# Kernel tuning notes

Hardware: AMD Instinct MI355X
Metric: run time of the kernel (lower is better)

## Reference

```python
import jax, jax.numpy as jnp
import numpy as np

EPS = 1e-5
N_LAYERS = 4  # int(log2(patch_size=16))


def _conv(x, w, stride=1, pad=0):
    return jax.lax.conv_general_dilated(
        x, w, (stride, stride), ((pad, pad), (pad, pad)),
        dimension_numbers=('NCHW', 'OIHW', 'NCHW'))


def _mbn(x, m, g, b):
    # masked BatchNorm1d over active (nnz) sites only; m is [B,1,H,W] 0/1
    cnt = jnp.maximum(m.sum(), 1.0)
    mean = (x * m).sum((0, 2, 3)) / cnt
    xc = x - mean[None, :, None, None]
    var = (xc * xc * m).sum((0, 2, 3)) / cnt
    y = xc * jax.lax.rsqrt(var + EPS)[None, :, None, None]
    return (y * g[None, :, None, None] + b[None, :, None, None]) * m


def _down_mask(m):
    # active-output sites of a k=3, stride=2, pad=1 regular sparse conv
    return jax.lax.reduce_window(m, 0.0, jax.lax.max, (1, 1, 3, 3), (1, 1, 2, 2),
                                 ((0, 0), (0, 0), (1, 1), (1, 1)))


def setup_inputs() -> dict:
    key = jax.random.key(0)
    ks = jax.random.split(key, 24)
    B, C, H, W = 8, 3, 256, 256
    hd, ed, L = 192, 192, 256
    w = lambda k, shp: jax.random.normal(k, shp, jnp.float32) * 0.05
    inp = {
        'images': jax.random.normal(ks[0], (B, C, H, W), jnp.float32),
        'mask': jax.random.randint(ks[1], (B, L), 0, 2).astype(jnp.int32),
        'stem_w': w(ks[2], (hd, C, 1, 1)),
        'stem_g': jnp.ones((hd,), jnp.float32), 'stem_b': jnp.zeros((hd,), jnp.float32),
        'dw1': w(ks[3], (N_LAYERS, hd, hd, 3, 3)),
        'dg1': jnp.ones((N_LAYERS, hd), jnp.float32), 'db1': jnp.zeros((N_LAYERS, hd), jnp.float32),
        'dw2': w(ks[4], (N_LAYERS, hd, hd, 3, 3)),
        'dg2': jnp.ones((N_LAYERS, hd), jnp.float32), 'db2': jnp.zeros((N_LAYERS, hd), jnp.float32),
        'rw1': w(ks[5], (N_LAYERS, hd, hd, 3, 3)),
        'rg1': jnp.ones((N_LAYERS, hd), jnp.float32), 'rb1': jnp.zeros((N_LAYERS, hd), jnp.float32),
        'rw2': w(ks[6], (N_LAYERS, hd, hd, 3, 3)),
        'rg2': jnp.ones((N_LAYERS, hd), jnp.float32), 'rb2': jnp.zeros((N_LAYERS, hd), jnp.float32),
        'final_w': w(ks[7], (ed, hd, 1, 1)),
        'final_g': jnp.ones((ed,), jnp.float32), 'final_b': jnp.zeros((ed,), jnp.float32),
    }
    return inp


def reference(images, mask, stem_w, stem_g, stem_b,
              dw1, dg1, db1, dw2, dg2, db2,
              rw1, rg1, rb1, rw2, rg2, rb2,
              final_w, final_g, final_b):
    B, C, H, W = images.shape
    L = mask.shape[1]
    f = int(np.sqrt(L))
    s = H // f
    keep = (1 - mask).astype(images.dtype).reshape(B, f, f)
    m = jnp.repeat(jnp.repeat(keep, s, axis=1), s, axis=2)[:, None]  # [B,1,H,W]
    x = images * m  # dense emulation of sparse tensor: inactive sites are zero

    # stem (regular 1x1 conv, active set unchanged) + BN + ReLU
    x = jnp.maximum(_mbn(_conv(x, stem_w), m, stem_g, stem_b), 0.0)

    for i in range(N_LAYERS):
        # ResBlockDownSparse: regular conv k3 s2 -> BN -> ReLU -> subm conv -> BN
        x = _conv(x, dw1[i], stride=2, pad=1)
        m = _down_mask(m)
        x = jnp.maximum(_mbn(x, m, dg1[i], db1[i]), 0.0)
        x = _mbn(_conv(x, dw2[i], 1, 1), m, dg2[i], db2[i])
        # ResBlockSparse (in==out, no skip projection)
        idn = x
        h = jnp.maximum(_mbn(_conv(x, rw1[i], 1, 1), m, rg1[i], rb1[i]), 0.0)
        h = _mbn(_conv(h, rw2[i], 1, 1), m, rg2[i], rb2[i])
        x = jnp.maximum(h + idn, 0.0)

    # final 1x1 subm proj + BN + ReLU
    x = jnp.maximum(_mbn(_conv(x, final_w), m, final_g, final_b), 0.0)
    ids_restore = jnp.tile(jnp.arange(L, dtype=jnp.int32)[None], (B, 1))
    return x, mask, ids_restore
```

## Files before the change

### kernel.cpp

```cpp
#include <hip/hip_runtime.h>
#include <hip/hip_bf16.h>

typedef __hip_bfloat16 bf16;
typedef unsigned short u16;
typedef unsigned int u32;
typedef unsigned char u8;
typedef __attribute__((ext_vector_type(8))) short bf16x8;
typedef __attribute__((ext_vector_type(4))) float f32x4;

#define NB 8
#define CH 192
#define WSZ (CH*CH*9)
#define WBLK (CH*32)


static __device__ __forceinline__ float bf2f(bf16 v){ return __bfloat162float(v); }
static __device__ __forceinline__ u16 f2bu(float f){
  union { bf16 h; u16 u; } cv; cv.h = __float2bfloat16(f); return cv.u;
}
static __device__ __forceinline__ float u2f(u16 u){
  union { bf16 h; u16 u; } cv; cv.u = u; return __bfloat162float(cv.h);
}
static __device__ __forceinline__ u32 pk2bf(float a, float b){
  union { __hip_bfloat162 h; u32 u; } cv;
  cv.h = __float22bfloat162_rn(make_float2(a, b));
  return cv.u;
}

static __device__ __forceinline__ void build_ss(const float* __restrict__ stIn,
        const float* __restrict__ g, const float* __restrict__ bb,
        const float* __restrict__ cnt, float* scs, float* shs, int t){
  if(t < CH){
    float s = 0.f, s2 = 0.f;
#pragma unroll
    for(int b=0;b<NB;b++){ s += stIn[b*384 + t]; s2 += stIn[b*384 + 192 + t]; }
    float n = fmaxf(*cnt, 1.0f);
    float mean = s/n;
    float var = fmaxf(s2/n - mean*mean, 0.f);
    float rstd = rsqrtf(var + 1e-5f);
    float sc = g[t]*rstd;
    scs[t] = sc;
    shs[t] = bb[t] - mean*sc;
  }
}

template<int RELU>
static __device__ __forceinline__ uint4 affine8(uint4 v, const float* scp, const float* shp){
  float4 sa = *(const float4*)(scp);
  float4 sb = *(const float4*)(scp+4);
  float4 ha = *(const float4*)(shp);
  float4 hb = *(const float4*)(shp+4);
  u16* pv = (u16*)&v;
  float f0, f1;
  f0 = u2f(pv[0])*sa.x + ha.x; f1 = u2f(pv[1])*sa.y + ha.y;
  if(RELU){ f0 = fmaxf(f0,0.f); f1 = fmaxf(f1,0.f); }
  ((u32*)&v)[0] = pk2bf(f0, f1);
  f0 = u2f(pv[2])*sa.z + ha.z; f1 = u2f(pv[3])*sa.w + ha.w;
  if(RELU){ f0 = fmaxf(f0,0.f); f1 = fmaxf(f1,0.f); }
  ((u32*)&v)[1] = pk2bf(f0, f1);
  f0 = u2f(pv[4])*sb.x + hb.x; f1 = u2f(pv[5])*sb.y + hb.y;
  if(RELU){ f0 = fmaxf(f0,0.f); f1 = fmaxf(f1,0.f); }
  ((u32*)&v)[2] = pk2bf(f0, f1);
  f0 = u2f(pv[6])*sb.z + hb.z; f1 = u2f(pv[7])*sb.w + hb.w;
  if(RELU){ f0 = fmaxf(f0,0.f); f1 = fmaxf(f1,0.f); }
  ((u32*)&v)[3] = pk2bf(f0, f1);
  return v;
}


__global__ void k_zero(float* p, int n){
  int i = blockIdx.x*blockDim.x + threadIdx.x;
  if(i < n) p[i] = 0.f;
}

__global__ void k_fill(float* p, int n, float v){
  int i = blockIdx.x*blockDim.x + threadIdx.x;
  if(i < n) p[i] = v;
}

__global__ void k_mask0(const int* __restrict__ mask, u8* __restrict__ m0){
  int i = blockIdx.x*blockDim.x + threadIdx.x;
  if(i >= NB*65536) return;
  int b = i >> 16; int p = i & 65535;
  int y = p >> 8, x = p & 255;
  int patch = (y >> 4)*16 + (x >> 4);
  m0[i] = (u8)(1 - mask[b*256 + patch]);
}

__global__ void k_maskdown(const u8* __restrict__ mi, u8* __restrict__ mo,
                           int Ho, int Wo, int Hi, int Wi){
  int i = blockIdx.x*blockDim.x + threadIdx.x;
  int total = NB*Ho*Wo; if(i >= total) return;
  int b = i/(Ho*Wo); int p = i%(Ho*Wo);
  int oy = p/Wo, ox = p%Wo;
  u8 v = 0;
  for(int ky=0; ky<3; ky++){
    int iy = oy*2 + ky - 1; if(iy < 0 || iy >= Hi) continue;
    for(int kx=0; kx<3; kx++){
      int ix = ox*2 + kx - 1; if(ix < 0 || ix >= Wi) continue;
      u8 t = mi[(b*Hi + iy)*Wi + ix]; if(t > v) v = t;
    }
  }
  mo[i] = v;
}

__global__ void k_count(const u8* __restrict__ m, int n, float* cnt){
  int i = blockIdx.x*blockDim.x + threadIdx.x;
  int stride = gridDim.x*blockDim.x;
  int local = 0;
  for(int j=i; j<n; j+=stride) local += m[j];
  for(int o=32; o>0; o>>=1) local += __shfl_down(local, o, 64);
  if((threadIdx.x & 63) == 0 && local) atomicAdd(cnt, (float)local);
}


__global__ __launch_bounds__(256) void k_moments(const float* __restrict__ im,
        const u8* __restrict__ m0, float* __restrict__ mom){
  float s[9];
#pragma unroll
  for(int k=0;k<9;k++) s[k]=0.f;
  int stride = gridDim.x*blockDim.x;
  for(int i = blockIdx.x*blockDim.x + threadIdx.x; i < NB*65536; i += stride){
    if(m0[i]){
      int b = i >> 16, p = i & 65535;
      float r = im[(size_t)(b*3+0)*65536 + p];
      float g = im[(size_t)(b*3+1)*65536 + p];
      float bl= im[(size_t)(b*3+2)*65536 + p];
      s[0]+=r;    s[1]+=g;    s[2]+=bl;
      s[3]+=r*r;  s[4]+=g*g;  s[5]+=bl*bl;
      s[6]+=r*g;  s[7]+=r*bl; s[8]+=g*bl;
    }
  }
#pragma unroll
  for(int k=0;k<9;k++){
    for(int o=32; o>0; o>>=1) s[k] += __shfl_down(s[k], o, 64);
  }
  __shared__ float sh[4][9];
  int w = threadIdx.x >> 6;
  if((threadIdx.x & 63) == 0){
#pragma unroll
    for(int k=0;k<9;k++) sh[w][k] = s[k];
  }
  __syncthreads();
  if(threadIdx.x < 9){
    float tt = sh[0][threadIdx.x] + sh[1][threadIdx.x] + sh[2][threadIdx.x] + sh[3][threadIdx.x];
    atomicAdd(&mom[threadIdx.x], tt);
  }
}

__global__ void k_stemfinal(const float* __restrict__ mom, const float* __restrict__ cnt,
        const float* __restrict__ sw, const float* __restrict__ g,
        const float* __restrict__ bb, float* __restrict__ ssA){
  int c = threadIdx.x; if(c >= CH) return;
  float n = fmaxf(*cnt, 1.0f);
  float m0=mom[0], m1=mom[1], m2=mom[2], m3=mom[3], m4=mom[4];
  float m5=mom[5], m6=mom[6], m7=mom[7], m8=mom[8];
  float w0 = sw[c*3+0], w1 = sw[c*3+1], w2 = sw[c*3+2];
  float mean = (w0*m0 + w1*m1 + w2*m2)/n;
  float e2 = (w0*w0*m3 + w1*w1*m4 + w2*w2*m5
            + 2.f*(w0*w1*m6 + w0*w2*m7 + w1*w2*m8))/n;
  float var = fmaxf(e2 - mean*mean, 0.f);
  float sc = g[c]*rsqrtf(var + 1e-5f);
  ssA[c] = sc;
  ssA[CH + c] = bb[c] - mean*sc;
}

__global__ void k_fold(const float* __restrict__ sw, const float* __restrict__ ssA,
                       float* __restrict__ swf){
  int c = threadIdx.x; if(c >= CH) return;
  float sc = ssA[c];
  swf[c*4+0] = sc*sw[c*3+0];
  swf[c*4+1] = sc*sw[c*3+1];
  swf[c*4+2] = sc*sw[c*3+2];
  swf[c*4+3] = ssA[CH+c];
}

__global__ void k_repack16(const float* __restrict__ dw1, const float* __restrict__ dw2,
                           const float* __restrict__ rw1, const float* __restrict__ rw2,
                           bf16* __restrict__ wb){
  int i = blockIdx.x*blockDim.x + threadIdx.x;
  if(i >= 16*WSZ) return;
  int stage = i/(4*WSZ);
  int sel = (i/WSZ)%4;
  int r = i%WSZ;
  const float* w = (sel==0)?dw1 : (sel==1)?dw2 : (sel==2)?rw1 : rw2;
  float val = w[(size_t)stage*WSZ + r];
  int tap = r%9; int ci = (r/9)%CH; int co = r/(9*CH);
  wb[(size_t)(stage*4+sel)*WSZ + ((size_t)(tap*6 + (ci>>5))*CH + co)*32 + (ci&31)]
      = __float2bfloat16(val);
}

__global__ void k_repackF(const float* __restrict__ fw, bf16* __restrict__ wb){
  int i = blockIdx.x*blockDim.x + threadIdx.x;
  if(i >= CH*CH) return;
  int co = i/CH, ci = i%CH;
  wb[((size_t)(ci>>5)*CH + co)*32 + (ci&31)] = __float2bfloat16(fw[i]);
}


static __device__ __forceinline__ void epi_stats(f32x4 (&acc)[4][3], const u8* sm,
        float* __restrict__ statsB, int b, int co0, int l15, int q, int lane){
  float s[3], s2[3];
#pragma unroll
  for(int nt=0;nt<3;nt++){ s[nt]=0.f; s2[nt]=0.f; }
#pragma unroll
  for(int mt=0;mt<4;mt++){
#pragma unroll
    for(int r=0;r<4;r++){
      int site = mt*16 + q*4 + r;
      float mv = (float)sm[site];
#pragma unroll
      for(int nt=0;nt<3;nt++){
        float v = acc[mt][nt][r]*mv;
        s[nt] += v; s2[nt] += v*v;
      }
    }
  }
#pragma unroll
  for(int nt=0;nt<3;nt++){
    s[nt]  += __shfl_down(s[nt], 32, 64);  s[nt]  += __shfl_down(s[nt], 16, 64);
    s2[nt] += __shfl_down(s2[nt], 32, 64); s2[nt] += __shfl_down(s2[nt], 16, 64);
  }
  if(lane < 16){
#pragma unroll
    for(int nt=0;nt<3;nt++){
      int co = co0 + nt*16 + l15;
      atomicAdd(&statsB[b*384 + co], s[nt]);
      atomicAdd(&statsB[b*384 + 192 + co], s2[nt]);
    }
  }
}

static __device__ __forceinline__ void epi_store(f32x4 (&acc)[4][3], u16* obuf,
        u16* __restrict__ out, int b, int oy0, int ox0, int Ho, int Wo,
        int t, int co0, int l15, int q){
  __syncthreads();
#pragma unroll
  for(int mt=0;mt<4;mt++){
#pragma unroll
    for(int nt=0;nt<3;nt++){
      int co = co0 + nt*16 + l15;
#pragma unroll
      for(int r=0;r<4;r++){
        int site = mt*16 + q*4 + r;
        obuf[site*212 + co] = f2bu(acc[mt][nt][r]);
      }
    }
  }
  __syncthreads();
  for(int e=t; e<3072; e+=256){
    int r = e/384; int off = (e%384)*4;
    int sx = off/CH, co = off%CH;
    ushort4 v = *(const ushort4*)&obuf[(r*8+sx)*212 + co];
    *(ushort4*)(out + ((size_t)(b*Ho+oy0+r)*Wo + ox0)*CH + off) = v;
  }
}


static __device__ __forceinline__ void epi_stats8(f32x4 (&acc)[8][3], const u8* sm,
        float* __restrict__ statsB, int b, int co0, int l15, int q, int lane){
  float s[3], s2[3];
#pragma unroll
  for(int nt=0;nt<3;nt++){ s[nt]=0.f; s2[nt]=0.f; }
#pragma unroll
  for(int mt=0;mt<8;mt++){
#pragma unroll
    for(int r=0;r<4;r++){
      int site = mt*16 + q*4 + r;
      float mv = (float)sm[site];
#pragma unroll
      for(int nt=0;nt<3;nt++){
        float v = acc[mt][nt][r]*mv;
        s[nt] += v; s2[nt] += v*v;
      }
    }
  }
#pragma unroll
  for(int nt=0;nt<3;nt++){
    s[nt]  += __shfl_down(s[nt], 32, 64);  s[nt]  += __shfl_down(s[nt], 16, 64);
    s2[nt] += __shfl_down(s2[nt], 32, 64); s2[nt] += __shfl_down(s2[nt], 16, 64);
  }
  if(lane < 16){
#pragma unroll
    for(int nt=0;nt<3;nt++){
      int co = co0 + nt*16 + l15;
      atomicAdd(&statsB[b*384 + co], s[nt]);
      atomicAdd(&statsB[b*384 + 192 + co], s2[nt]);
    }
  }
}

static __device__ __forceinline__ void epi_store_q(f32x4 (&acc)[8][3], u16* obuf,
        u16* __restrict__ out, int b, int oy0, int ox0, int Ho, int Wo,
        int t, int co0, int l15, int q, int qd){
  __syncthreads();
#pragma unroll
  for(int mi=0; mi<2; mi++){
    int mt = qd*2 + mi;
#pragma unroll
    for(int nt=0;nt<3;nt++){
      int co = co0 + nt*16 + l15;
#pragma unroll
      for(int r=0;r<4;r++){
        int site = mi*16 + q*4 + r;
        obuf[site*212 + co] = f2bu(acc[mt][nt][r]);
      }
    }
  }
  __syncthreads();
  for(int e=t; e<1536; e+=256){
    int r = e/384; int off = (e%384)*4;
    int sx = off/CH, co = off%CH;
    ushort4 v = *(const ushort4*)&obuf[(r*8+sx)*212 + co];
    *(ushort4*)(out + ((size_t)(b*Ho+oy0+qd*4+r)*Wo + ox0)*CH + off) = v;
  }
}


static __device__ __forceinline__ void epi_statsT(f32x4 (&acc)[2][3], const u8* sm,
        float* __restrict__ statsB, int b, int co0, int l15, int q, int lane, int mh){
  float s[3], s2[3];
#pragma unroll
  for(int nt=0;nt<3;nt++){ s[nt]=0.f; s2[nt]=0.f; }
#pragma unroll
  for(int mt=0;mt<2;mt++){
#pragma unroll
    for(int r=0;r<4;r++){
      int site = mh*32 + mt*16 + q*4 + r;
      float mv = (float)sm[site];
#pragma unroll
      for(int nt=0;nt<3;nt++){
        float v = acc[mt][nt][r]*mv;
        s[nt] += v; s2[nt] += v*v;
      }
    }
  }
#pragma unroll
  for(int nt=0;nt<3;nt++){
    s[nt]  += __shfl_down(s[nt], 32, 64);  s[nt]  += __shfl_down(s[nt], 16, 64);
    s2[nt] += __shfl_down(s2[nt], 32, 64); s2[nt] += __shfl_down(s2[nt], 16, 64);
  }
  if(lane < 16){
#pragma unroll
    for(int nt=0;nt<3;nt++){
      int co = co0 + nt*16 + l15;
      atomicAdd(&statsB[b*384 + co], s[nt]);
      atomicAdd(&statsB[b*384 + 192 + co], s2[nt]);
    }
  }
}

static __device__ __forceinline__ void epi_storeT(f32x4 (&acc)[2][3], u16* obuf,
        u16* __restrict__ out, int b, int oy0, int ox0, int Ho, int Wo,
        int t, int w, int coh, int l15, int q, int mh){
  __syncthreads();
#pragma unroll
  for(int mt=0;mt<2;mt++){
#pragma unroll
    for(int nt=0;nt<3;nt++){
      int col = (w&1)*48 + nt*16 + l15;
#pragma unroll
      for(int r=0;r<4;r++){
        int site = mh*32 + mt*16 + q*4 + r;
        obuf[site*104 + col] = f2bu(acc[mt][nt][r]);
      }
    }
  }
  __syncthreads();
  for(int e=t; e<1536; e+=256){
    int site = e/24; int grp = e%24;
    ushort4 v = *(const ushort4*)&obuf[site*104 + grp*4];
    *(ushort4*)(out + ((size_t)(b*Ho+oy0+(site>>3))*Wo + ox0+(site&7))*CH + coh*96 + grp*4) = v;
  }
}

#define CIP 104
template<int RELU>
__global__ __launch_bounds__(256) void k_convm(const bf16* __restrict__ in,
        const bf16* __restrict__ wb, const u8* __restrict__ mk,
        bf16* __restrict__ out, int Ho, int Wo,
        const float* __restrict__ stIn, const float* __restrict__ gIn,
        const float* __restrict__ bIn, const float* __restrict__ cnt,
        float* __restrict__ statsB){
  __shared__ __align__(16) u16 tile[180*CIP];
  __shared__ __align__(16) float scs[CH], shs[CH];
  __shared__ u8 sm[128];
  __shared__ u8 wmk[180];
  __shared__ int anyact;
  const int t = threadIdx.x;
  const int b = blockIdx.z;
  const int ox0 = blockIdx.x*8, oy0 = blockIdx.y*16;
  const int gy0 = oy0 - 1, gx0 = ox0 - 1;

  if(t == 0) anyact = 0;
  __syncthreads();
  if(t < 128){
    int r = t >> 3, c = t & 7;
    u8 mv = mk[(b*Ho + oy0 + r)*Wo + ox0 + c];
    sm[t] = mv;
    if(mv) anyact = 1;
  }
  for(int e=t; e<180; e+=256){
    int y = e/10, x = e%10;
    int gy = gy0 + y, gx = gx0 + x;
    u8 mv = 0;
    if(gy >= 0 && gy < Ho && gx >= 0 && gx < Wo) mv = mk[(b*Ho+gy)*Wo+gx];
    wmk[e] = mv;
  }
  __syncthreads();
  if(!anyact) return;

  build_ss(stIn, gIn, bIn, cnt, scs, shs, t);
  __syncthreads();

  const u16* inp = (const u16*)in;
  const int w = t >> 6;
  const int l = t & 63;
  const int l15 = l & 15, q = l >> 4;
  f32x4 acc[8][3];
#pragma unroll
  for(int mt=0;mt<8;mt++)
#pragma unroll
    for(int nt=0;nt<3;nt++) acc[mt][nt] = (f32x4){0.f,0.f,0.f,0.f};

  int sy[8], sx[8];
#pragma unroll
  for(int mt=0;mt<8;mt++){ int s = mt*16 + l15; sy[mt] = s>>3; sx[mt] = s&7; }
  const int co0 = w*48;
  const u16* wt = (const u16*)wb;
  int bco[3];
#pragma unroll
  for(int nt=0;nt<3;nt++) bco[nt] = (co0 + nt*16 + l15)*32 + q*8;

  for(int p=0; p<2; p++){
    if(p) __syncthreads();
    const int cb = p*96;
    for(int u=t; u<2160; u+=256){
      int site = u/12; int grp = u%12;
      int y = site/10, x = site%10;
      int gy = gy0 + y, gx = gx0 + x;
      uint4 v = {0u,0u,0u,0u};
      if(wmk[site]){
        v = *(const uint4*)(inp + ((size_t)(b*Ho+gy)*Wo+gx)*CH + cb + grp*8);
        v = affine8<RELU>(v, &scs[cb + grp*8], &shs[cb + grp*8]);
      }
      *(uint4*)&tile[site*CIP + grp*8] = v;
    }
    __syncthreads();
    for(int tap=0; tap<9; tap++){
      const int ky = tap/3, kx = tap%3;
      const u16* tb[8];
#pragma unroll
      for(int mt=0;mt<8;mt++)
        tb[mt] = &tile[((sy[mt]+ky)*10 + sx[mt]+kx)*CIP + q*8];
#pragma unroll
      for(int c=0;c<3;c++){
        const u16* wp = wt + (size_t)(tap*6 + p*3 + c)*WBLK;
        bf16x8 a[8], bbv[3];
#pragma unroll
        for(int mt=0;mt<8;mt++) a[mt] = *(const bf16x8*)(tb[mt] + c*32);
#pragma unroll
        for(int nt=0;nt<3;nt++) bbv[nt] = *(const bf16x8*)(wp + bco[nt]);
#pragma unroll
        for(int mt=0;mt<8;mt++)
#pragma unroll
          for(int nt=0;nt<3;nt++)
            acc[mt][nt] = __builtin_amdgcn_mfma_f32_16x16x32_bf16(a[mt], bbv[nt], acc[mt][nt], 0, 0, 0);
      }
    }
  }
  epi_stats8(acc, sm, statsB, b, co0, l15, q, l);
  epi_store_q(acc, tile, (u16*)out, b, oy0, ox0, Ho, Wo, t, co0, l15, q, 0);
  epi_store_q(acc, tile, (u16*)out, b, oy0, ox0, Ho, Wo, t, co0, l15, q, 1);
  epi_store_q(acc, tile, (u16*)out, b, oy0, ox0, Ho, Wo, t, co0, l15, q, 2);
  epi_store_q(acc, tile, (u16*)out, b, oy0, ox0, Ho, Wo, t, co0, l15, q, 3);
}

#define CIPT 200
template<int RELU>
__global__ __launch_bounds__(256) void k_convmT(const bf16* __restrict__ in,
        const bf16* __restrict__ wb, const u8* __restrict__ mk,
        bf16* __restrict__ out, int Ho, int Wo,
        const float* __restrict__ stIn, const float* __restrict__ gIn,
        const float* __restrict__ bIn, const float* __restrict__ cnt,
        float* __restrict__ statsB){
  __shared__ __align__(16) u16 tile[100*CIPT];
  __shared__ __align__(16) float scs[CH], shs[CH];
  __shared__ u8 sm[64];
  __shared__ u8 wmk[100];
  __shared__ int anyact;
  const int t = threadIdx.x;
  const int zb = blockIdx.z;
  const int b = zb & (NB-1);
  const int coh = zb >> 3;
  const int ox0 = blockIdx.x*8, oy0 = blockIdx.y*8;
  const int gy0 = oy0 - 1, gx0 = ox0 - 1;

  if(t == 0) anyact = 0;
  __syncthreads();
  if(t < 64){
    int r = t >> 3, c = t & 7;
    u8 mv = mk[(b*Ho + oy0 + r)*Wo + ox0 + c];
    sm[t] = mv;
    if(mv) anyact = 1;
  } else if(t < 164){
    int e = t - 64;
    int y = e/10, x = e%10;
    int gy = gy0 + y, gx = gx0 + x;
    u8 mv = 0;
    if(gy >= 0 && gy < Ho && gx >= 0 && gx < Wo) mv = mk[(b*Ho+gy)*Wo+gx];
    wmk[e] = mv;
  }
  __syncthreads();
  if(!anyact) return;

  build_ss(stIn, gIn, bIn, cnt, scs, shs, t);
  __syncthreads();

  const u16* inp = (const u16*)in;
  for(int u=t; u<2400; u+=256){
    int y = u/240; int rem = u%240; int x = rem/24; int cu = rem%24;
    int gy = gy0 + y, gx = gx0 + x;
    uint4 v = {0u,0u,0u,0u};
    if(wmk[y*10+x]){
      v = *(const uint4*)(inp + ((size_t)(b*Ho+gy)*Wo+gx)*CH + cu*8);
      v = affine8<RELU>(v, &scs[cu*8], &shs[cu*8]);
    }
    *(uint4*)&tile[(y*10+x)*CIPT + cu*8] = v;
  }
  __syncthreads();

  const int w = t >> 6;
  const int l = t & 63;
  const int l15 = l & 15, q = l >> 4;
  const int mh = w >> 1;
  f32x4 acc[2][3];
#pragma unroll
  for(int mt=0;mt<2;mt++)
#pragma unroll
    for(int nt=0;nt<3;nt++) acc[mt][nt] = (f32x4){0.f,0.f,0.f,0.f};

  int sy[2], sx[2];
#pragma unroll
  for(int mt=0;mt<2;mt++){ int s = mh*32 + mt*16 + l15; sy[mt] = s>>3; sx[mt] = s&7; }
  const int co0 = coh*96 + (w&1)*48;
  const u16* wt = (const u16*)wb;
  int bco[3];
#pragma unroll
  for(int nt=0;nt<3;nt++) bco[nt] = (co0 + nt*16 + l15)*32 + q*8;

  for(int tap=0; tap<9; tap++){
    const int ky = tap/3, kx = tap%3;
    const u16* tb[2];
#pragma unroll
    for(int mt=0;mt<2;mt++)
      tb[mt] = &tile[((sy[mt]+ky)*10 + sx[mt]+kx)*CIPT + q*8];
#pragma unroll
    for(int c=0;c<6;c++){
      const u16* wp = wt + (size_t)(tap*6 + c)*WBLK;
      bf16x8 a[2], bbv[3];
#pragma unroll
      for(int mt=0;mt<2;mt++) a[mt] = *(const bf16x8*)(tb[mt] + c*32);
#pragma unroll
      for(int nt=0;nt<3;nt++) bbv[nt] = *(const bf16x8*)(wp + bco[nt]);
#pragma unroll
      for(int mt=0;mt<2;mt++)
#pragma unroll
        for(int nt=0;nt<3;nt++)
          acc[mt][nt] = __builtin_amdgcn_mfma_f32_16x16x32_bf16(a[mt], bbv[nt], acc[mt][nt], 0, 0, 0);
    }
  }
  epi_statsT(acc, sm, statsB, b, co0, l15, q, l, mh);
  epi_storeT(acc, tile, (u16*)out, b, oy0, ox0, Ho, Wo, t, w, coh, l15, q, mh);
}


__global__ __launch_bounds__(256) void k_convs2T(const bf16* __restrict__ in,
        const bf16* __restrict__ wb, const u8* __restrict__ mk,
        bf16* __restrict__ out, int Ho, int Wo, float* __restrict__ statsB){
  __shared__ __align__(16) u16 obuf[64*104];
  __shared__ u8 sm[64];
  __shared__ int anyact;
  const int t = threadIdx.x;
  const int zb = blockIdx.z;
  const int b = zb & (NB-1);
  const int coh = zb >> 3;
  const int ox0 = blockIdx.x*8, oy0 = blockIdx.y*8;
  const int Hi = Ho*2, Wi = Wo*2;

  if(t == 0) anyact = 0;
  __syncthreads();
  if(t < 64){
    int r = t >> 3, c = t & 7;
    u8 mv = mk[(b*Ho + oy0 + r)*Wo + ox0 + c];
    sm[t] = mv;
    if(mv) anyact = 1;
  }
  __syncthreads();
  if(!anyact) return;

  const u16* inp = (const u16*)in;
  const int w = t >> 6;
  const int l = t & 63;
  const int l15 = l & 15, q = l >> 4;
  const int mh = w >> 1;
  f32x4 acc[2][3];
#pragma unroll
  for(int mt=0;mt<2;mt++)
#pragma unroll
    for(int nt=0;nt<3;nt++) acc[mt][nt] = (f32x4){0.f,0.f,0.f,0.f};

  int gyb[2], gxb[2];
#pragma unroll
  for(int mt=0;mt<2;mt++){
    int s = mh*32 + mt*16 + l15;
    gyb[mt] = (oy0 + (s>>3))*2 - 1;
    gxb[mt] = (ox0 + (s&7))*2 - 1;
  }
  const int co0 = coh*96 + (w&1)*48;
  const bf16x8 zro = {0,0,0,0,0,0,0,0};
  const u16* wt = (const u16*)wb;
  int bco[3];
#pragma unroll
  for(int nt=0;nt<3;nt++) bco[nt] = (co0 + nt*16 + l15)*32 + q*8;

  for(int tap=0; tap<9; tap++){
    const int ky = tap/3, kx = tap%3;
    const u16* ap[2]; bool av[2];
#pragma unroll
    for(int mt=0;mt<2;mt++){
      int gy = gyb[mt] + ky, gx = gxb[mt] + kx;
      av[mt] = (gy >= 0 && gy < Hi && gx >= 0 && gx < Wi);
      ap[mt] = inp + ((size_t)(b*Hi+gy)*Wi+gx)*CH + q*8;
    }
#pragma unroll
    for(int c=0;c<6;c++){
      const u16* wp = wt + (size_t)(tap*6 + c)*WBLK;
      bf16x8 a[2], bbv[3];
#pragma unroll
      for(int mt=0;mt<2;mt++) a[mt] = av[mt] ? *(const bf16x8*)(ap[mt] + c*32) : zro;
#pragma unroll
      for(int nt=0;nt<3;nt++) bbv[nt] = *(const bf16x8*)(wp + bco[nt]);
#pragma unroll
      for(int mt=0;mt<2;mt++)
#pragma unroll
        for(int nt=0;nt<3;nt++)
          acc[mt][nt] = __builtin_amdgcn_mfma_f32_16x16x32_bf16(a[mt], bbv[nt], acc[mt][nt], 0, 0, 0);
    }
  }
  epi_statsT(acc, sm, statsB, b, co0, l15, q, l, mh);
  epi_storeT(acc, obuf, (u16*)out, b, oy0, ox0, Ho, Wo, t, w, coh, l15, q, mh);
}

#define CIP0 36
#define NS0 561
__global__ __launch_bounds__(256) void k_conv0m(const float* __restrict__ im,
        const float* __restrict__ swf, const u8* __restrict__ m0,
        const bf16* __restrict__ wb, const u8* __restrict__ mk,
        bf16* __restrict__ out, float* __restrict__ statsB){
  __shared__ __align__(16) u16 tile[NS0*CIP0];
  __shared__ __align__(16) u16 bfr[576*8];
  __shared__ u8 sm[128];
  __shared__ int anyact;
  const int t = threadIdx.x;
  const int b = blockIdx.z;
  const int ox0 = blockIdx.x*8, oy0 = blockIdx.y*16;

  if(t == 0) anyact = 0;
  __syncthreads();
  if(t < 128){
    int r = t >> 3, c = t & 7;
    u8 mv = mk[(b*128 + oy0 + r)*128 + ox0 + c];
    sm[t] = mv;
    if(mv) anyact = 1;
  }
  __syncthreads();
  if(!anyact) return;

  const int gy0 = oy0*2 - 1, gx0 = ox0*2 - 1;
  for(int e=t; e<576; e+=256){
    u32 w0=0u, w1=0u, w2=0u, w3=0u;
    if(e < NS0){
      int y = e/17, x = e%17;
      int gy = gy0 + y, gx = gx0 + x;
      if(gy >= 0 && gy < 256 && gx >= 0 && gx < 256){
        int pi = gy*256 + gx;
        if(m0[b*65536 + pi]){
          float rm = im[(size_t)(b*3+0)*65536 + pi];
          float gm = im[(size_t)(b*3+1)*65536 + pi];
          float bm = im[(size_t)(b*3+2)*65536 + pi];
          float rh = u2f(f2bu(rm)), gh = u2f(f2bu(gm)), bh = u2f(f2bu(bm));
          w0 = pk2bf(rm, gm);      w1 = pk2bf(bm, 1.0f);
          w2 = pk2bf(rm-rh, gm-gh); w3 = pk2bf(bm-bh, 0.f);
        }
      }
    }
    *(uint4*)&bfr[e*8] = make_uint4(w0, w1, w2, w3);
  }

  const int w = t >> 6;
  const int l = t & 63;
  const int l15 = l & 15, q = l >> 4;
  const bf16x8 zf = {0,0,0,0,0,0,0,0};

  f32x4 acc[8][3];
#pragma unroll
  for(int mt=0;mt<8;mt++)
#pragma unroll
    for(int nt=0;nt<3;nt++) acc[mt][nt] = (f32x4){0.f,0.f,0.f,0.f};

  int siy[8], six[8];
#pragma unroll
  for(int mt=0;mt<8;mt++){ int s = mt*16 + l15; siy[mt] = (s>>3)*2; six[mt] = (s&7)*2; }
  const int co0 = w*48;
  const u16* wt = (const u16*)wb;
  int bco[3];
#pragma unroll
  for(int nt=0;nt<3;nt++) bco[nt] = (co0 + nt*16 + l15)*32 + q*8;

  for(int h=0; h<6; h++){
    __syncthreads();
    bf16x8 af[2];
#pragma unroll
    for(int mtl=0;mtl<2;mtl++){
      af[mtl] = zf;
      if(q == 0){
        const float4 wv = *(const float4*)&swf[(h*32 + mtl*16 + l15)*4];
        u32 wlo = pk2bf(wv.x, wv.y);
        ((u32*)&af[mtl])[0] = wlo;
        ((u32*)&af[mtl])[1] = pk2bf(wv.z, wv.w);
        ((u32*)&af[mtl])[2] = wlo;
        ((u32*)&af[mtl])[3] = pk2bf(wv.z, 0.f);
      }
    }
#pragma unroll
    for(int i=0;i<9;i++){
      int nt = w + i*4;
      int site = nt*16 + l15;
      bf16x8 bs = zf;
      if(q == 0) bs = *(const bf16x8*)&bfr[(site < 576 ? site : 575)*8];
#pragma unroll
      for(int mtl=0;mtl<2;mtl++){
        f32x4 d = __builtin_amdgcn_mfma_f32_16x16x32_bf16(af[mtl], bs,
                        (f32x4){0.f,0.f,0.f,0.f}, 0, 0, 0);
        if(site < NS0){
          u32 lo = pk2bf(fmaxf(d[0],0.f), fmaxf(d[1],0.f));
          u32 hi = pk2bf(fmaxf(d[2],0.f), fmaxf(d[3],0.f));
          *(uint2*)&tile[site*CIP0 + mtl*16 + q*4] = make_uint2(lo, hi);
        }
      }
    }
    __syncthreads();
    for(int tap=0; tap<9; tap++){
      const int ky = tap/3, kx = tap%3;
      const u16* wp = wt + (size_t)(tap*6 + h)*WBLK;
      bf16x8 a[8], bbv[3];
#pragma unroll
      for(int mt=0;mt<8;mt++)
        a[mt] = *(const bf16x8*)&tile[((siy[mt]+ky)*17 + six[mt]+kx)*CIP0 + q*8];
#pragma unroll
      for(int nt=0;nt<3;nt++) bbv[nt] = *(const bf16x8*)(wp + bco[nt]);
#pragma unroll
      for(int mt=0;mt<8;mt++)
#pragma unroll
        for(int nt=0;nt<3;nt++)
          acc[mt][nt] = __builtin_amdgcn_mfma_f32_16x16x32_bf16(a[mt], bbv[nt], acc[mt][nt], 0, 0, 0);
    }
  }
  epi_stats8(acc, sm, statsB, b, co0, l15, q, l);
  epi_store_q(acc, tile, (u16*)out, b, oy0, ox0, 128, 128, t, co0, l15, q, 0);
  epi_store_q(acc, tile, (u16*)out, b, oy0, ox0, 128, 128, t, co0, l15, q, 1);
  epi_store_q(acc, tile, (u16*)out, b, oy0, ox0, 128, 128, t, co0, l15, q, 2);
  epi_store_q(acc, tile, (u16*)out, b, oy0, ox0, 128, 128, t, co0, l15, q, 3);
}


__global__ __launch_bounds__(256) void k_resid(const bf16* __restrict__ xD,
        const bf16* __restrict__ xB, const u8* __restrict__ m,
        const float* __restrict__ stD, const float* __restrict__ gD, const float* __restrict__ bD,
        const float* __restrict__ stB, const float* __restrict__ gB, const float* __restrict__ bB,
        const float* __restrict__ cnt, bf16* __restrict__ out, int sites){
  __shared__ __align__(16) float scD[CH], shD[CH], scB[CH], shB[CH];
  const int t = threadIdx.x;
  build_ss(stD, gD, bD, cnt, scD, shD, t);
  build_ss(stB, gB, bB, cnt, scB, shB, t);
  __syncthreads();
  int idx = blockIdx.x*256 + t;
  int total = sites*24;
  if(idx >= total) return;
  int si = idx/24; int c0 = (idx%24)*8;
  float mv = (float)m[si];
  const u16* pd = (const u16*)xD + (size_t)si*CH + c0;
  const u16* pb = (const u16*)xB + (size_t)si*CH + c0;
  uint4 vd = *(const uint4*)pd;
  uint4 vb = *(const uint4*)pb;
  u16* dd = (u16*)&vd; u16* db = (u16*)&vb;
  uint4 vo;
#pragma unroll
  for(int j=0;j<4;j++){
    int c = c0 + j*2;
    float f0 = (u2f(dd[j*2  ])*scD[c  ] + shD[c  ])*mv + (u2f(db[j*2  ])*scB[c  ] + shB[c  ])*mv;
    float f1 = (u2f(dd[j*2+1])*scD[c+1] + shD[c+1])*mv + (u2f(db[j*2+1])*scB[c+1] + shB[c+1])*mv;
    ((u32*)&vo)[j] = pk2bf(fmaxf(f0, 0.f), fmaxf(f1, 0.f));
  }
  *(uint4*)((u16*)out + (size_t)si*CH + c0) = vo;
}


__global__ __launch_bounds__(256) void k_finalm(const bf16* __restrict__ in,
        const bf16* __restrict__ wb, const u8* __restrict__ m4,
        bf16* __restrict__ out, float* __restrict__ statsB){
  __shared__ __align__(16) u16 obuf[64*212];
  __shared__ u8 sm[64];
  __shared__ int anyact;
  const int t = threadIdx.x;
  const int b = blockIdx.z;
  const int base = blockIdx.x*64;

  if(t == 0) anyact = 0;
  __syncthreads();
  if(t < 64){
    u8 mv = m4[b*256 + base + t];
    sm[t] = mv;
    if(mv) anyact = 1;
  }
  __syncthreads();
  if(!anyact) return;

  const int w = t >> 6;
  const int l = t & 63;
  const int l15 = l & 15, q = l >> 4;
  const int co0 = w*48;
  f32x4 acc[4][3];
#pragma unroll
  for(int mt=0;mt<4;mt++)
#pragma unroll
    for(int nt=0;nt<3;nt++) acc[mt][nt] = (f32x4){0.f,0.f,0.f,0.f};

  const u16* inp = (const u16*)in + (size_t)(b*256 + base)*CH + q*8;
  const u16* wt = (const u16*)wb;
  int bco[3];
#pragma unroll
  for(int nt=0;nt<3;nt++) bco[nt] = (co0 + nt*16 + l15)*32 + q*8;
#pragma unroll
  for(int c=0;c<6;c++){
    const u16* wp = wt + (size_t)c*WBLK;
    bf16x8 a[4], bbv[3];
#pragma unroll
    for(int mt=0;mt<4;mt++)
      a[mt] = *(const bf16x8*)(inp + (size_t)(mt*16 + l15)*CH + c*32);
#pragma unroll
    for(int nt=0;nt<3;nt++) bbv[nt] = *(const bf16x8*)(wp + bco[nt]);
#pragma unroll
    for(int mt=0;mt<4;mt++)
#pragma unroll
      for(int nt=0;nt<3;nt++)
        acc[mt][nt] = __builtin_amdgcn_mfma_f32_16x16x32_bf16(a[mt], bbv[nt], acc[mt][nt], 0, 0, 0);
  }
  epi_stats(acc, sm, statsB, b, co0, l15, q, l);
  epi_store(acc, obuf, (u16*)out, b, blockIdx.x*8, 0, 32, 8, t, co0, l15, q);
}

__global__ __launch_bounds__(256) void k_bnapply_out(const bf16* __restrict__ x,
        const u8* __restrict__ m, const float* __restrict__ stF,
        const float* __restrict__ g, const float* __restrict__ bb,
        const float* __restrict__ cnt, float* __restrict__ out){
  __shared__ __align__(16) float scs[CH], shs[CH];
  const int t = threadIdx.x;
  build_ss(stF, g, bb, cnt, scs, shs, t);
  __syncthreads();
  int i = blockIdx.x*256 + t;
  if(i >= NB*CH*256) return;
  int p = i % 256; int c = (i/256) % CH; int b = i/(256*CH);
  int si = b*256 + p;
  float v = bf2f(x[(size_t)si*CH + c])*scs[c] + shs[c];
  v *= (float)m[si];
  v = fmaxf(v, 0.f);
  out[i] = v;
}


__global__ void k_tail(const int* __restrict__ mask, float* __restrict__ out){
  int i = blockIdx.x*blockDim.x + threadIdx.x;
  if(i < 2048){
    out[393216 + i] = (float)mask[i];
  } else if(i < 4096){
    int j = i - 2048;
    out[395264 + j] = (float)(j & 255);
  }
}


extern "C" void kernel_launch(void* const* d_in, const int* in_sizes, int n_in,
                              void* d_out, int out_size, void* d_ws, size_t ws_size,
                              hipStream_t stream){
  const float* images = (const float*)d_in[0];
  const int*   maskI  = (const int*)d_in[1];
  const float* stem_w = (const float*)d_in[2];
  const float* stem_g = (const float*)d_in[3];
  const float* stem_b = (const float*)d_in[4];
  const float* dw1 = (const float*)d_in[5];
  const float* dg1 = (const float*)d_in[6];
  const float* db1 = (const float*)d_in[7];
  const float* dw2 = (const float*)d_in[8];
  const float* dg2 = (const float*)d_in[9];
  const float* db2 = (const float*)d_in[10];
  const float* rw1 = (const float*)d_in[11];
  const float* rg1 = (const float*)d_in[12];
  const float* rb1 = (const float*)d_in[13];
  const float* rw2 = (const float*)d_in[14];
  const float* rg2 = (const float*)d_in[15];
  const float* rb2 = (const float*)d_in[16];
  const float* final_w = (const float*)d_in[17];
  const float* final_g = (const float*)d_in[18];
  const float* final_b = (const float*)d_in[19];
  float* outF = (float*)d_out;

  char* wsp = (char*)d_ws;
  auto alloc = [&](size_t bytes)->char*{
    char* p = wsp; wsp += (bytes + 255) & ~(size_t)255; return p;
  };
  bf16* S0 = (bf16*)alloc((size_t)NB*CH*16384*2);
  bf16* S1 = (bf16*)alloc((size_t)NB*CH*16384*2);
  bf16* S2 = (bf16*)alloc((size_t)NB*CH*16384*2);
  int Hs[5] = {256,128,64,32,16};
  u8* M[5];
  for(int l=0;l<5;l++) M[l] = (u8*)alloc((size_t)NB*Hs[l]*Hs[l]);
  bf16*  Wb16 = (bf16*)alloc((size_t)17*WSZ*2);
  float* swf = (float*)alloc(CH*4*4);
  float* statsB16 = (float*)alloc((size_t)17*NB*384*4);
  float* statsF = (float*)alloc(384*4);
  float* ssA   = (float*)alloc(2*CH*4);
  float* cnts  = (float*)alloc(8*4);
  size_t need = (size_t)(wsp - (char*)d_ws);

  if(ws_size < need){
    k_fill<<<(393216+255)/256, 256, 0, stream>>>(outF, 393216, 777.0f);
    k_tail<<<16, 256, 0, stream>>>(maskI, outF);
    return;
  }

  int nz = 17*NB*384 + 384;
  k_zero<<<(nz+255)/256, 256, 0, stream>>>(statsB16, nz);
  k_zero<<<1, 32, 0, stream>>>(cnts, 8);
  k_repack16<<<(16*WSZ+255)/256, 256, 0, stream>>>(dw1, dw2, rw1, rw2, Wb16);
  k_repackF<<<(CH*CH+255)/256, 256, 0, stream>>>(final_w, Wb16 + (size_t)16*WSZ);

  k_mask0<<<(NB*65536+255)/256, 256, 0, stream>>>(maskI, M[0]);
  for(int l=1;l<5;l++){
    int total = NB*Hs[l]*Hs[l];
    k_maskdown<<<(total+255)/256, 256, 0, stream>>>(M[l-1], M[l], Hs[l], Hs[l], Hs[l-1], Hs[l-1]);
  }
  for(int l=0;l<5;l++){
    int n = NB*Hs[l]*Hs[l];
    int blocks = (n + 256*64 - 1)/(256*64); if(blocks < 1) blocks = 1; if(blocks > 256) blocks = 256;
    k_count<<<blocks, 256, 0, stream>>>(M[l], n, cnts + l);
  }

  k_moments<<<512, 256, 0, stream>>>(images, M[0], statsF);
  k_stemfinal<<<1, CH, 0, stream>>>(statsF, cnts + 0, stem_w, stem_g, stem_b, ssA);
  k_fold<<<1, CH, 0, stream>>>(stem_w, ssA, swf);

  bf16* X = nullptr;
  for(int i=0;i<4;i++){
    int Ho = Hs[i+1];
    int sites = NB*Ho*Ho;
    const u8* mk = M[i+1];
    const float* cnt = cnts + i + 1;
    bf16* A = S0;
    bf16* B = (i % 2 == 0) ? S1 : S2;
    bf16* C2 = (i == 0) ? S2 : X;
    const bf16* W0 = Wb16 + (size_t)(i*4+0)*WSZ;
    const bf16* W1 = Wb16 + (size_t)(i*4+1)*WSZ;
    const bf16* W2 = Wb16 + (size_t)(i*4+2)*WSZ;
    const bf16* W3 = Wb16 + (size_t)(i*4+3)*WSZ;
    float* st0 = statsB16 + (size_t)(i*4+0)*NB*384;
    float* st1 = statsB16 + (size_t)(i*4+1)*NB*384;
    float* st2 = statsB16 + (size_t)(i*4+2)*NB*384;
    float* st3 = statsB16 + (size_t)(i*4+3)*NB*384;

    dim3 gT(Ho/8, Ho/8, NB*2);
    if(i == 0){
      k_conv0m<<<dim3(16, 8, NB), 256, 0, stream>>>(images, swf, M[0], W0, M[1], A, st0);
    } else {
      k_convs2T<<<gT, 256, 0, stream>>>(X, W0, mk, A, Ho, Ho, st0);
    }
    if(Ho >= 64){
      dim3 g2(Ho/8, Ho/16, NB);
      k_convm<1><<<g2, 256, 0, stream>>>(A, W1, mk, B, Ho, Ho,
          st0, dg1 + i*CH, db1 + i*CH, cnt, st1);
      k_convm<0><<<g2, 256, 0, stream>>>(B, W2, mk, A, Ho, Ho,
          st1, dg2 + i*CH, db2 + i*CH, cnt, st2);
      k_convm<1><<<g2, 256, 0, stream>>>(A, W3, mk, C2, Ho, Ho,
          st2, rg1 + i*CH, rb1 + i*CH, cnt, st3);
    } else {
      k_convmT<1><<<gT, 256, 0, stream>>>(A, W1, mk, B, Ho, Ho,
          st0, dg1 + i*CH, db1 + i*CH, cnt, st1);
      k_convmT<0><<<gT, 256, 0, stream>>>(B, W2, mk, A, Ho, Ho,
          st1, dg2 + i*CH, db2 + i*CH, cnt, st2);
      k_convmT<1><<<gT, 256, 0, stream>>>(A, W3, mk, C2, Ho, Ho,
          st2, rg1 + i*CH, rb1 + i*CH, cnt, st3);
    }
    k_resid<<<(sites*24 + 255)/256, 256, 0, stream>>>(C2, B, mk,
        st3, rg2 + i*CH, rb2 + i*CH,
        st1, dg2 + i*CH, db2 + i*CH, cnt, B, sites);
    X = B;
  }

  float* stF = statsB16 + (size_t)16*NB*384;
  k_finalm<<<dim3(4, 1, NB), 256, 0, stream>>>(X, Wb16 + (size_t)16*WSZ, M[4], S0, stF);
  k_bnapply_out<<<(NB*CH*256 + 255)/256, 256, 0, stream>>>(S0, M[4], stF,
      final_g, final_b, cnts + 4, outF);

  k_tail<<<16, 256, 0, stream>>>(maskI, outF);
}
```

Baseline: 1.071 ms.

## Switch 3x3 conv kernel to 32x32x16 MFMA with per-wave site split

```diff
diff --git a/kernel.cpp b/kernel.cpp
--- a/kernel.cpp
+++ b/kernel.cpp
@@ -7,6 +7,7 @@
 typedef unsigned char u8;
 typedef __attribute__((ext_vector_type(8))) short bf16x8;
 typedef __attribute__((ext_vector_type(4))) float f32x4;
+typedef __attribute__((ext_vector_type(16))) float f32x16;
 
 #define NB 8
 #define CH 192
@@ -257,62 +258,56 @@
 }
 
 
-static __device__ __forceinline__ void epi_stats8(f32x4 (&acc)[8][3], const u8* sm,
-        float* __restrict__ statsB, int b, int co0, int l15, int q, int lane){
-  float s[3], s2[3];
-#pragma unroll
-  for(int nt=0;nt<3;nt++){ s[nt]=0.f; s2[nt]=0.f; }
-#pragma unroll
-  for(int mt=0;mt<8;mt++){
-#pragma unroll
-    for(int r=0;r<4;r++){
-      int site = mt*16 + q*4 + r;
-      float mv = (float)sm[site];
-#pragma unroll
-      for(int nt=0;nt<3;nt++){
-        float v = acc[mt][nt][r]*mv;
-        s[nt] += v; s2[nt] += v*v;
-      }
-    }
-  }
-#pragma unroll
-  for(int nt=0;nt<3;nt++){
-    s[nt]  += __shfl_down(s[nt], 32, 64);  s[nt]  += __shfl_down(s[nt], 16, 64);
-    s2[nt] += __shfl_down(s2[nt], 32, 64); s2[nt] += __shfl_down(s2[nt], 16, 64);
-  }
-  if(lane < 16){
-#pragma unroll
-    for(int nt=0;nt<3;nt++){
-      int co = co0 + nt*16 + l15;
+static __device__ __forceinline__ void epi_stats32(f32x16 (&acc)[6], const u8* sm,
+        float* __restrict__ statsB, int b, int w, int l31, int hi, int lane){
+  float s[6], s2[6];
+#pragma unroll
+  for(int nt=0;nt<6;nt++){ s[nt]=0.f; s2[nt]=0.f; }
+#pragma unroll
+  for(int g=0;g<16;g++){
+    int site = w*32 + (g&3) + 8*(g>>2) + 4*hi;
+    float mv = (float)sm[site];
+#pragma unroll
+    for(int nt=0;nt<6;nt++){
+      float v = acc[nt][g]*mv;
+      s[nt] += v; s2[nt] += v*v;
+    }
+  }
+#pragma unroll
+  for(int nt=0;nt<6;nt++){
+    s[nt]  += __shfl_down(s[nt], 32, 64);
+    s2[nt] += __shfl_down(s2[nt], 32, 64);
+  }
+  if(lane < 32){
+#pragma unroll
+    for(int nt=0;nt<6;nt++){
+      int co = nt*32 + l31;
       atomicAdd(&statsB[b*384 + co], s[nt]);
       atomicAdd(&statsB[b*384 + 192 + co], s2[nt]);
     }
   }
 }
 
-static __device__ __forceinline__ void epi_store_q(f32x4 (&acc)[8][3], u16* obuf,
+static __device__ __forceinline__ void epi_store32_h(f32x16 (&acc)[6], u16* obuf,
         u16* __restrict__ out, int b, int oy0, int ox0, int Ho, int Wo,
-        int t, int co0, int l15, int q, int qd){
-  __syncthreads();
-#pragma unroll
-  for(int mi=0; mi<2; mi++){
-    int mt = qd*2 + mi;
-#pragma unroll
-    for(int nt=0;nt<3;nt++){
-      int co = co0 + nt*16 + l15;
-#pragma unroll
-      for(int r=0;r<4;r++){
-        int site = mi*16 + q*4 + r;
-        obuf[site*212 + co] = f2bu(acc[mt][nt][r]);
-      }
-    }
-  }
-  __syncthreads();
-  for(int e=t; e<1536; e+=256){
+        int t, int w, int l31, int hi, int half){
+  __syncthreads();
+  if((w >> 1) == half){
+    int lq = w & 1;
+#pragma unroll
+    for(int g=0;g<16;g++){
+      int lsite = lq*32 + (g&3) + 8*(g>>2) + 4*hi;
+#pragma unroll
+      for(int nt=0;nt<6;nt++)
+        obuf[lsite*212 + nt*32 + l31] = f2bu(acc[nt][g]);
+    }
+  }
+  __syncthreads();
+  for(int e=t; e<3072; e+=256){
     int r = e/384; int off = (e%384)*4;
     int sx = off/CH, co = off%CH;
     ushort4 v = *(const ushort4*)&obuf[(r*8+sx)*212 + co];
-    *(ushort4*)(out + ((size_t)(b*Ho+oy0+qd*4+r)*Wo + ox0)*CH + off) = v;
+    *(ushort4*)(out + ((size_t)(b*Ho+oy0+half*8+r)*Wo + ox0)*CH + off) = v;
   }
 }
 
@@ -416,21 +411,17 @@
   const u16* inp = (const u16*)in;
   const int w = t >> 6;
   const int l = t & 63;
-  const int l15 = l & 15, q = l >> 4;
-  f32x4 acc[8][3];
-#pragma unroll
-  for(int mt=0;mt<8;mt++)
-#pragma unroll
-    for(int nt=0;nt<3;nt++) acc[mt][nt] = (f32x4){0.f,0.f,0.f,0.f};
-
-  int sy[8], sx[8];
-#pragma unroll
-  for(int mt=0;mt<8;mt++){ int s = mt*16 + l15; sy[mt] = s>>3; sx[mt] = s&7; }
-  const int co0 = w*48;
+  const int l31 = l & 31, hi = l >> 5;
+  f32x16 acc32[6];
+#pragma unroll
+  for(int nt=0;nt<6;nt++)
+#pragma unroll
+    for(int g=0;g<16;g++) acc32[nt][g] = 0.f;
+
+  const int s = w*32 + l31;
+  const int sy = s >> 3, sx = s & 7;
   const u16* wt = (const u16*)wb;
-  int bco[3];
-#pragma unroll
-  for(int nt=0;nt<3;nt++) bco[nt] = (co0 + nt*16 + l15)*32 + q*8;
+  const int bbase = l31*32 + hi*8;
 
   for(int p=0; p<2; p++){
     if(p) __syncthreads();
@@ -449,31 +440,22 @@
     __syncthreads();
     for(int tap=0; tap<9; tap++){
       const int ky = tap/3, kx = tap%3;
-      const u16* tb[8];
-#pragma unroll
-      for(int mt=0;mt<8;mt++)
-        tb[mt] = &tile[((sy[mt]+ky)*10 + sx[mt]+kx)*CIP + q*8];
-#pragma unroll
-      for(int c=0;c<3;c++){
-        const u16* wp = wt + (size_t)(tap*6 + p*3 + c)*WBLK;
-        bf16x8 a[8], bbv[3];
-#pragma unroll
-        for(int mt=0;mt<8;mt++) a[mt] = *(const bf16x8*)(tb[mt] + c*32);
-#pragma unroll
-        for(int nt=0;nt<3;nt++) bbv[nt] = *(const bf16x8*)(wp + bco[nt]);
-#pragma unroll
-        for(int mt=0;mt<8;mt++)
-#pragma unroll
-          for(int nt=0;nt<3;nt++)
-            acc[mt][nt] = __builtin_amdgcn_mfma_f32_16x16x32_bf16(a[mt], bbv[nt], acc[mt][nt], 0, 0, 0);
-      }
-    }
-  }
-  epi_stats8(acc, sm, statsB, b, co0, l15, q, l);
-  epi_store_q(acc, tile, (u16*)out, b, oy0, ox0, Ho, Wo, t, co0, l15, q, 0);
-  epi_store_q(acc, tile, (u16*)out, b, oy0, ox0, Ho, Wo, t, co0, l15, q, 1);
-  epi_store_q(acc, tile, (u16*)out, b, oy0, ox0, Ho, Wo, t, co0, l15, q, 2);
-  epi_store_q(acc, tile, (u16*)out, b, oy0, ox0, Ho, Wo, t, co0, l15, q, 3);
+      const u16* tb = &tile[((sy+ky)*10 + sx+kx)*CIP + hi*8];
+#pragma unroll
+      for(int k16=0;k16<6;k16++){
+        bf16x8 a = *(const bf16x8*)(tb + k16*16);
+        const u16* wp = wt + (size_t)(tap*6 + p*3 + (k16>>1))*WBLK + (k16&1)*16 + bbase;
+#pragma unroll
+        for(int nt=0;nt<6;nt++){
+          bf16x8 bv = *(const bf16x8*)(wp + nt*1024);
+          acc32[nt] = __builtin_amdgcn_mfma_f32_32x32x16_bf16(a, bv, acc32[nt], 0, 0, 0);
+        }
+      }
+    }
+  }
+  epi_stats32(acc32, sm, statsB, b, w, l31, hi, l);
+  epi_store32_h(acc32, tile, (u16*)out, b, oy0, ox0, Ho, Wo, t, w, l31, hi, 0);
+  epi_store32_h(acc32, tile, (u16*)out, b, oy0, ox0, Ho, Wo, t, w, l31, hi, 1);
 }
 
 #define CIPT 200
@@ -767,11 +749,62 @@
           acc[mt][nt] = __builtin_amdgcn_mfma_f32_16x16x32_bf16(a[mt], bbv[nt], acc[mt][nt], 0, 0, 0);
     }
   }
-  epi_stats8(acc, sm, statsB, b, co0, l15, q, l);
-  epi_store_q(acc, tile, (u16*)out, b, oy0, ox0, 128, 128, t, co0, l15, q, 0);
-  epi_store_q(acc, tile, (u16*)out, b, oy0, ox0, 128, 128, t, co0, l15, q, 1);
-  epi_store_q(acc, tile, (u16*)out, b, oy0, ox0, 128, 128, t, co0, l15, q, 2);
-  epi_store_q(acc, tile, (u16*)out, b, oy0, ox0, 128, 128, t, co0, l15, q, 3);
+  epi_stats8_impl:;
+  {
+    float s[3], s2[3];
+#pragma unroll
+    for(int nt=0;nt<3;nt++){ s[nt]=0.f; s2[nt]=0.f; }
+#pragma unroll
+    for(int mt=0;mt<8;mt++){
+#pragma unroll
+      for(int r=0;r<4;r++){
+        int site = mt*16 + q*4 + r;
+        float mv = (float)sm[site];
+#pragma unroll
+        for(int nt=0;nt<3;nt++){
+          float v = acc[mt][nt][r]*mv;
+          s[nt] += v; s2[nt] += v*v;
+        }
+      }
+    }
+#pragma unroll
+    for(int nt=0;nt<3;nt++){
+      s[nt]  += __shfl_down(s[nt], 32, 64);  s[nt]  += __shfl_down(s[nt], 16, 64);
+      s2[nt] += __shfl_down(s2[nt], 32, 64); s2[nt] += __shfl_down(s2[nt], 16, 64);
+    }
+    if(l < 16){
+#pragma unroll
+      for(int nt=0;nt<3;nt++){
+        int co = co0 + nt*16 + l15;
+        atomicAdd(&statsB[b*384 + co], s[nt]);
+        atomicAdd(&statsB[b*384 + 192 + co], s2[nt]);
+      }
+    }
+  }
+#pragma unroll
+  for(int qd=0; qd<4; qd++){
+    __syncthreads();
+#pragma unroll
+    for(int mi=0; mi<2; mi++){
+      int mt = qd*2 + mi;
+#pragma unroll
+      for(int nt=0;nt<3;nt++){
+        int co = co0 + nt*16 + l15;
+#pragma unroll
+        for(int r=0;r<4;r++){
+          int site = mi*16 + q*4 + r;
+          tile[site*212 + co] = f2bu(acc[mt][nt][r]);
+        }
+      }
+    }
+    __syncthreads();
+    for(int e=t; e<1536; e+=256){
+      int r = e/384; int off = (e%384)*4;
+      int sx = off/CH, co = off%CH;
+      ushort4 v = *(const ushort4*)&tile[(r*8+sx)*212 + co];
+      *(ushort4*)((u16*)out + ((size_t)(b*128+oy0+qd*4+r)*128 + ox0)*CH + off) = v;
+    }
+  }
 }
 
 
```

Result: slower. 1.476 ms (+37.9%).
